# Kernel optimization log

Hardware: AMD Instinct MI355X
Metric: run time of the kernel (lower is better)

Reference implementation:

```python
import jax, jax.numpy as jnp
import numpy as np

EPS = 1e-6
H = 8        # num_heads
DH = 64      # head dim = embed_dim // num_heads
LN_EPS = 1e-5


def _layernorm(x, g, b):
    m = jnp.mean(x, axis=-1, keepdims=True)
    v = jnp.mean(jnp.square(x - m), axis=-1, keepdims=True)
    return (x - m) / jnp.sqrt(v + LN_EPS) * g + b


def _flow_attention(x, Wq, bq, Wk, bk, Wv, bv, Wo, bo):
    # Non-causal Flow-Attention (Flowformer): kernelized sigmoid Q/K,
    # flow-conservation sink/source normalization, linear-attention kv trick.
    B, L, D = x.shape
    S = L
    q = jax.nn.sigmoid((x @ Wq + bq).reshape(B, L, H, DH).transpose(0, 2, 1, 3))  # bhld
    k = jax.nn.sigmoid((x @ Wk + bk).reshape(B, S, H, DH).transpose(0, 2, 1, 3))
    v = (x @ Wv + bv).reshape(B, S, H, DH).transpose(0, 2, 1, 3)

    sink_incoming = 1.0 / jnp.einsum('nhld,nhd->nhl', q + EPS, k.sum(axis=2) + EPS)
    source_outgoing = 1.0 / jnp.einsum('nhld,nhd->nhl', k + EPS, q.sum(axis=2) + EPS)
    conserved_sink = jnp.einsum('nhld,nhd->nhl', q + EPS,
                                (k * source_outgoing[..., None]).sum(axis=2) + EPS)
    conserved_source = jnp.einsum('nhld,nhd->nhl', k + EPS,
                                  (q * sink_incoming[..., None]).sum(axis=2) + EPS)
    conserved_source = jnp.clip(conserved_source, -1.0, 1.0)
    sink_allocation = jax.nn.sigmoid(conserved_sink * (float(L) / float(S)))
    source_competition = jax.nn.softmax(conserved_source, axis=-1) * float(S)

    # linear attention: kv = k^T (v * comp), out = (q * sink_in) kv
    kv = jnp.einsum('nhld,nhlm->nhdm', k, v * source_competition[..., None])
    o = jnp.einsum('nhld,nhdm->nhlm', q * sink_incoming[..., None], kv)
    o = o * sink_allocation[..., None]
    o = o.transpose(0, 2, 1, 3).reshape(B, L, D)
    return o @ Wo + bo


def setup_inputs() -> dict:
    key = jax.random.key(0)
    ks = jax.random.split(key, 16)
    B, L, D, F = 2, 16384, 512, 2048
    s = 0.02
    inp = {
        'x': jax.random.normal(ks[0], (B, L, D), dtype=jnp.float32),
        'Wq': jax.random.normal(ks[1], (D, D), dtype=jnp.float32) * s,
        'bq': jnp.zeros((D,), jnp.float32),
        'Wk': jax.random.normal(ks[2], (D, D), dtype=jnp.float32) * s,
        'bk': jnp.zeros((D,), jnp.float32),
        'Wv': jax.random.normal(ks[3], (D, D), dtype=jnp.float32) * s,
        'bv': jnp.zeros((D,), jnp.float32),
        'Wo': jax.random.normal(ks[4], (D, D), dtype=jnp.float32) * s,
        'bo': jnp.zeros((D,), jnp.float32),
        'W1': jax.random.normal(ks[5], (D, F), dtype=jnp.float32) * s,
        'b1': jnp.zeros((F,), jnp.float32),
        'W2': jax.random.normal(ks[6], (F, D), dtype=jnp.float32) * s,
        'b2': jnp.zeros((D,), jnp.float32),
        'g1': jnp.ones((D,), jnp.float32),
        'be1': jnp.zeros((D,), jnp.float32),
        'g2': jnp.ones((D,), jnp.float32),
        'be2': jnp.zeros((D,), jnp.float32),
    }
    return inp


def reference(x, Wq, bq, Wk, bk, Wv, bv, Wo, bo, W1, b1, W2, b2, g1, be1, g2, be2):
    # norm_first FlowformerLayer. NOTE: original _sa_block returns
    # dropout(attn(x))[0, :, :] -> [L, D], broadcast-added over batch (faithful).
    sa = _flow_attention(_layernorm(x, g1, be1), Wq, bq, Wk, bk, Wv, bv, Wo, bo)[0]
    x = x + sa  # [B,L,D] + [L,D]
    h = _layernorm(x, g2, be2)
    h = jax.nn.gelu(h @ W1 + b1, approximate=False) @ W2 + b2
    return x + h
```

## Files before the change

### kernel.cpp

```cpp
#include <hip/hip_runtime.h>
#include <hip/hip_bf16.h>
#include <cstdint>
#include <cstddef>


#define L_SEQ 16384
#define EPSF 1e-6f

typedef __bf16 b16x8 __attribute__((ext_vector_type(8)));
typedef __bf16 b16x4 __attribute__((ext_vector_type(4)));
typedef float  f32x4 __attribute__((ext_vector_type(4)));

#define FENCE() asm volatile("" ::: "memory")
#define BARF()  { FENCE(); __builtin_amdgcn_s_barrier(); FENCE(); }
#define WAITV(n) asm volatile("s_waitcnt vmcnt(" #n ")" ::: "memory")

__device__ __forceinline__ void gload16(const void* g, void* l) {
  __builtin_amdgcn_global_load_lds((const __attribute__((address_space(1))) void*)g,
                                   (__attribute__((address_space(3))) void*)l, 16, 0, 0);
}

__device__ __forceinline__ float sigmoidf_(float x) { return 1.f / (1.f + __expf(-x)); }

__global__ __launch_bounds__(256) void convT(const float* __restrict__ src,
                                             __bf16* __restrict__ dst, int K, int N) {
  __shared__ float tile[32][33];
  const int k0 = blockIdx.y * 32, n0 = blockIdx.x * 32;
  const int tx = threadIdx.x & 31, ty = threadIdx.x >> 5;
#pragma unroll
  for (int i = 0; i < 32; i += 8) tile[ty + i][tx] = src[(size_t)(k0 + ty + i) * N + n0 + tx];
  __syncthreads();
#pragma unroll
  for (int i = 0; i < 32; i += 8)
    dst[(size_t)(n0 + ty + i) * K + k0 + tx] = (__bf16)tile[tx][ty + i];
}

__global__ __launch_bounds__(256) void biascat_k(const float* __restrict__ bq,
                                                 const float* __restrict__ bk,
                                                 const float* __restrict__ bv,
                                                 float* __restrict__ bc) {
  int i = blockIdx.x * 256 + threadIdx.x;
  bc[i] = (i < 512) ? bq[i] : (i < 1024) ? bk[i - 512] : bv[i - 1024];
}

__global__ __launch_bounds__(256) void zero_k(float* __restrict__ p, int n) {
  int i = blockIdx.x * 256 + threadIdx.x;
  if (i < n) p[i] = 0.f;
}

__global__ __launch_bounds__(128) void ln_rows(const float* __restrict__ x,
                                               const float* __restrict__ g,
                                               const float* __restrict__ be,
                                               __bf16* __restrict__ out) {
  const int row = blockIdx.x, t = threadIdx.x;
  const float4 xv = reinterpret_cast<const float4*>(x + (size_t)row * 512)[t];
  float s = xv.x + xv.y + xv.z + xv.w;
  float s2 = xv.x * xv.x + xv.y * xv.y + xv.z * xv.z + xv.w * xv.w;
#pragma unroll
  for (int off = 32; off > 0; off >>= 1) { s += __shfl_down(s, off); s2 += __shfl_down(s2, off); }
  __shared__ float red[4];
  if ((t & 63) == 0) { red[(t >> 6) * 2] = s; red[(t >> 6) * 2 + 1] = s2; }
  __syncthreads();
  const float S = red[0] + red[2], S2 = red[1] + red[3];
  const float mean = S * (1.f / 512.f);
  const float var = S2 * (1.f / 512.f) - mean * mean;
  const float inv = rsqrtf(var + 1e-5f);
  const float4 gv = reinterpret_cast<const float4*>(g)[t];
  const float4 bv = reinterpret_cast<const float4*>(be)[t];
  b16x4 o;
  o[0] = (__bf16)((xv.x - mean) * inv * gv.x + bv.x);
  o[1] = (__bf16)((xv.y - mean) * inv * gv.y + bv.y);
  o[2] = (__bf16)((xv.z - mean) * inv * gv.z + bv.z);
  o[3] = (__bf16)((xv.w - mean) * inv * gv.w + bv.w);
  reinterpret_cast<b16x4*>(out + (size_t)row * 512)[t] = o;
}

__global__ __launch_bounds__(128) void x2ln2_k(const float* __restrict__ x,
                                               const float* __restrict__ sa0,
                                               const float* __restrict__ sa1,
                                               const float* __restrict__ bo,
                                               const float* __restrict__ g,
                                               const float* __restrict__ be,
                                               float* __restrict__ xout,
                                               __bf16* __restrict__ lnout) {
  const int row = blockIdx.x, t = threadIdx.x;
  const int l = row & (L_SEQ - 1);
  float4 xv = reinterpret_cast<const float4*>(x + (size_t)row * 512)[t];
  const float4 s0 = reinterpret_cast<const float4*>(sa0 + (size_t)l * 512)[t];
  const float4 s1 = reinterpret_cast<const float4*>(sa1 + (size_t)l * 512)[t];
  const float4 bb = reinterpret_cast<const float4*>(bo)[t];
  xv.x += s0.x + s1.x + bb.x; xv.y += s0.y + s1.y + bb.y;
  xv.z += s0.z + s1.z + bb.z; xv.w += s0.w + s1.w + bb.w;
  reinterpret_cast<float4*>(xout + (size_t)row * 512)[t] = xv;
  float s = xv.x + xv.y + xv.z + xv.w;
  float s2 = xv.x * xv.x + xv.y * xv.y + xv.z * xv.z + xv.w * xv.w;
#pragma unroll
  for (int off = 32; off > 0; off >>= 1) { s += __shfl_down(s, off); s2 += __shfl_down(s2, off); }
  __shared__ float red[4];
  if ((t & 63) == 0) { red[(t >> 6) * 2] = s; red[(t >> 6) * 2 + 1] = s2; }
  __syncthreads();
  const float S = red[0] + red[2], S2 = red[1] + red[3];
  const float mean = S * (1.f / 512.f);
  const float var = S2 * (1.f / 512.f) - mean * mean;
  const float inv = rsqrtf(var + 1e-5f);
  const float4 gv = reinterpret_cast<const float4*>(g)[t];
  const float4 bv = reinterpret_cast<const float4*>(be)[t];
  b16x4 o;
  o[0] = (__bf16)((xv.x - mean) * inv * gv.x + bv.x);
  o[1] = (__bf16)((xv.y - mean) * inv * gv.y + bv.y);
  o[2] = (__bf16)((xv.z - mean) * inv * gv.z + bv.z);
  o[3] = (__bf16)((xv.w - mean) * inv * gv.w + bv.w);
  reinterpret_cast<b16x4*>(lnout + (size_t)row * 512)[t] = o;
}

template <int EPI, int KSPL>
__global__ __launch_bounds__(256, 4) void gemm128(const __bf16* __restrict__ A,
                                                  const __bf16* __restrict__ Bt,
                                                  const int M, const int N, const int K,
                                                  const float* __restrict__ bias,
                                                  float* __restrict__ f0,
                                                  __bf16* __restrict__ h0,
                                                  __bf16* __restrict__ h1,
                                                  float* __restrict__ f1,
                                                  float* __restrict__ f2) {
  __shared__ alignas(16) __bf16 lds[16384];

  if constexpr (KSPL) {
    const int z = blockIdx.y;
    A += (size_t)z * (K >> 1);
    Bt += (size_t)z * (K >> 1);
    f0 += (size_t)z * ((size_t)M * N);
  }
  const int nt = KSPL ? (K >> 6) : (K >> 5);

  const int nwg = gridDim.x;
  const int orig = blockIdx.x;
  const int cpx = nwg >> 3;
  const int wg = (orig & 7) * cpx + (orig >> 3);
  const int gx = N >> 7;
  const int bm = (wg / gx) << 7;
  const int bn = (wg % gx) << 7;

  const int t = threadIdx.x;
  const int w = t >> 6, lane = t & 63;
  const int wr = w >> 1, wc = w & 1;
  const int fr = lane & 15;
  const int kb = lane >> 4;

  const __bf16* As = A + (size_t)(bm + (t >> 2)) * K + (t & 3) * 8;
  const __bf16* Bs = Bt + (size_t)(bn + (t >> 2)) * K + (t & 3) * 8;

  f32x4 acc[4][4] = {};

  auto STG = [&](int s) {
    const int sel = (s & 1) * 4096;
    const __bf16* ap = As + (s << 5);
    const __bf16* bp = Bs + (s << 5);
    gload16(ap, &lds[sel + t * 8]);
    gload16(ap + (size_t)64 * K, &lds[sel + 2048 + t * 8]);
    gload16(bp, &lds[8192 + sel + t * 8]);
    gload16(bp + (size_t)64 * K, &lds[8192 + sel + 2048 + t * 8]);
  };

  STG(0);
  WAITV(0);
  BARF();

  for (int s = 0; s < nt; s++) {
    if (s + 1 < nt) STG(s + 1);
    const int ab = (s & 1) * 4096 + (wr * 64 + fr) * 32 + kb * 8;
    const int bb2 = 8192 + (s & 1) * 4096 + (wc * 64 + fr) * 32 + kb * 8;
    b16x8 av[4], bv[4];
#pragma unroll
    for (int m = 0; m < 4; m++)
      av[m] = *reinterpret_cast<const b16x8*>(&lds[ab + m * 512]);
#pragma unroll
    for (int n = 0; n < 4; n++)
      bv[n] = *reinterpret_cast<const b16x8*>(&lds[bb2 + n * 512]);
#pragma unroll
    for (int m = 0; m < 4; m++)
#pragma unroll
      for (int n = 0; n < 4; n++)
        acc[m][n] = __builtin_amdgcn_mfma_f32_16x16x32_bf16(av[m], bv[n], acc[m][n], 0, 0, 0);
    WAITV(0);
    BARF();
  }

  const int r0 = kb * 4;
  const int cc = fr;
  if constexpr (EPI == 0) {
    const int which = bn >> 9;
    float cs[4] = {0.f, 0.f, 0.f, 0.f};
#pragma unroll
    for (int m = 0; m < 4; m++) {
#pragma unroll
      for (int n = 0; n < 4; n++) {
        const int col = bn + wc * 64 + n * 16 + cc;
        const int c2 = col & 511;
#pragma unroll
        for (int r = 0; r < 4; r++) {
          const int row = bm + wr * 64 + m * 16 + r0 + r;
          float val = acc[m][n][r] + bias[col];
          if (which < 2) {
            val = sigmoidf_(val);
            cs[n] += val;
            ((which == 0) ? h0 : h1)[(size_t)row * 512 + c2] = (__bf16)val;
          } else {
            f0[(size_t)row * 512 + c2] = val;
          }
        }
      }
    }
    if (which < 2) {
      float* sums = (which == 0) ? f1 : f2;
#pragma unroll
      for (int n = 0; n < 4; n++) {
        float s = cs[n];
        s += __shfl_xor(s, 16);
        s += __shfl_xor(s, 32);
        if (kb == 0) atomicAdd(&sums[(bn & 511) + wc * 64 + n * 16 + cc], s);
      }
    }
  } else {
#pragma unroll
    for (int m = 0; m < 4; m++) {
#pragma unroll
      for (int n = 0; n < 4; n++) {
        const int col = bn + wc * 64 + n * 16 + cc;
#pragma unroll
        for (int r = 0; r < 4; r++) {
          const int row = bm + wr * 64 + m * 16 + r0 + r;
          float val = acc[m][n][r];
          if constexpr (EPI == 1) {
            f0[(size_t)row * N + col] = val;
          } else if constexpr (EPI == 2) {
            const float xg = val + bias[col];
            const float gel = 0.5f * xg * (1.f + erff(xg * 0.70710678118f));
            h0[(size_t)row * N + col] = (__bf16)gel;
          } else {
            const size_t idx = (size_t)row * N + col;
            f0[idx] = f0[idx] + val + bias[col];
          }
        }
      }
    }
  }
}

__global__ __launch_bounds__(256) void attn_pass1(const __bf16* __restrict__ q,
                                                  const __bf16* __restrict__ k,
                                                  const float* __restrict__ qsum,
                                                  const float* __restrict__ ksum,
                                                  float* __restrict__ si_out,
                                                  float* __restrict__ qkpart) {
  __shared__ float lsQ[512], lsK[512];
  const int t = threadIdx.x, lane = t & 63, wv = t >> 6;
  const int c0 = lane * 8;
  lsQ[t] = 0.f; lsQ[t + 256] = 0.f;
  lsK[t] = 0.f; lsK[t + 256] = 0.f;
  __syncthreads();
  float qs[8], ks[8];
#pragma unroll
  for (int j = 0; j < 8; j++) {
    qs[j] = qsum[c0 + j] + EPSF;
    ks[j] = ksum[c0 + j] + EPSF;
  }
  const int h = lane >> 3;
  float qacc[8] = {}, kacc[8] = {};
#pragma unroll 1
  for (int i = 0; i < 8; i++) {
    const int l = blockIdx.x * 32 + wv * 8 + i;
    const b16x8 q8 = *reinterpret_cast<const b16x8*>(q + (size_t)l * 512 + c0);
    const b16x8 k8 = *reinterpret_cast<const b16x8*>(k + (size_t)l * 512 + c0);
    float qf[8], kf[8];
    float p1 = 0.f, p2 = 0.f;
#pragma unroll
    for (int j = 0; j < 8; j++) {
      qf[j] = (float)q8[j]; kf[j] = (float)k8[j];
      p1 += (qf[j] + EPSF) * ks[j];
      p2 += (kf[j] + EPSF) * qs[j];
    }
    p1 += __shfl_xor(p1, 1); p2 += __shfl_xor(p2, 1);
    p1 += __shfl_xor(p1, 2); p2 += __shfl_xor(p2, 2);
    p1 += __shfl_xor(p1, 4); p2 += __shfl_xor(p2, 4);
    const float siv = 1.f / p1, sov = 1.f / p2;
    if ((lane & 7) == 0) si_out[h * L_SEQ + l] = siv;
#pragma unroll
    for (int j = 0; j < 8; j++) { qacc[j] += qf[j] * siv; kacc[j] += kf[j] * sov; }
  }
#pragma unroll
  for (int j = 0; j < 8; j++) {
    atomicAdd(&lsQ[c0 + j], qacc[j]);
    atomicAdd(&lsK[c0 + j], kacc[j]);
  }
  __syncthreads();
  float* qp = qkpart + (size_t)blockIdx.x * 1024;
  qp[t] = lsQ[t];
  qp[t + 256] = lsQ[t + 256];
  qp[t + 512] = lsK[t];
  qp[t + 768] = lsK[t + 256];
}

__global__ __launch_bounds__(256) void reduce_qk(const float* __restrict__ qkpart,
                                                 float* __restrict__ outv) {
  const int i = blockIdx.x * 256 + threadIdx.x;
  float s = 0.f;
#pragma unroll 4
  for (int b = 0; b < 512; b++) s += qkpart[(size_t)b * 1024 + i];
  outv[i] = s;
}

__global__ __launch_bounds__(256) void kv_part(const __bf16* __restrict__ k,
                                               const float* __restrict__ v,
                                               const float* __restrict__ qsi,
                                               float* __restrict__ kvpart,
                                               float* __restrict__ separt) {
  const int h = blockIdx.y, bx = blockIdx.x, t = threadIdx.x;
  __shared__ float lsK[64 * 68];
  __shared__ float lsV[64 * 68];
  __shared__ float lsRed[256];
  const int r = t >> 2, cq = (t & 3) * 16;
  float qv[16];
#pragma unroll
  for (int j = 0; j < 16; j++) qv[j] = qsi[h * 64 + cq + j] + EPSF;
  const int d = t & 63, mg = t >> 6;
  f32x4 acc4[4] = {};
  float seloc = 0.f;
#pragma unroll 1
  for (int sc = 0; sc < 4; sc++) {
    const int l = bx * 256 + sc * 64 + r;
    __syncthreads();
    const b16x8 k8a = *reinterpret_cast<const b16x8*>(k + (size_t)l * 512 + h * 64 + cq);
    const b16x8 k8b = *reinterpret_cast<const b16x8*>(k + (size_t)l * 512 + h * 64 + cq + 8);
    f32x4 v4[4];
#pragma unroll
    for (int jj = 0; jj < 4; jj++)
      v4[jj] = *reinterpret_cast<const f32x4*>(v + (size_t)l * 512 + h * 64 + cq + jj * 4);
    float kf[16];
#pragma unroll
    for (int j = 0; j < 8; j++) { kf[j] = (float)k8a[j]; kf[8 + j] = (float)k8b[j]; }
    float p = 0.f;
#pragma unroll
    for (int j = 0; j < 16; j++) p += (kf[j] + EPSF) * qv[j];
    p += __shfl_xor(p, 1);
    p += __shfl_xor(p, 2);
    p = fminf(fmaxf(p, -1.f), 1.f);
    const float ce = __expf(p);
    if ((t & 3) == 0) seloc += ce;
#pragma unroll
    for (int j = 0; j < 16; j++) lsK[r * 68 + cq + j] = kf[j];
#pragma unroll
    for (int jj = 0; jj < 4; jj++)
      *reinterpret_cast<f32x4*>(&lsV[r * 68 + cq + jj * 4]) = v4[jj] * ce;
    __syncthreads();
    for (int rr = 0; rr < 64; rr++) {
      const float kd = lsK[rr * 68 + d];
      const f32x4* lv = reinterpret_cast<const f32x4*>(&lsV[rr * 68 + mg * 16]);
#pragma unroll
      for (int jj = 0; jj < 4; jj++) acc4[jj] += lv[jj] * kd;
    }
  }
  float* kp = kvpart + ((size_t)h * 64 + bx) * 4096;
#pragma unroll
  for (int jj = 0; jj < 4; jj++)
    *reinterpret_cast<f32x4*>(&kp[d * 64 + mg * 16 + jj * 4]) = acc4[jj];
  lsRed[t] = ((t & 3) == 0) ? seloc : 0.f;
  __syncthreads();
  for (int s2 = 128; s2 > 0; s2 >>= 1) {
    if (t < s2) lsRed[t] += lsRed[t + s2];
    __syncthreads();
  }
  if (t == 0) separt[h * 64 + bx] = lsRed[0];
}

__global__ __launch_bounds__(256) void kv_reduce(const float* __restrict__ kvpart,
                                                 const float* __restrict__ separt,
                                                 float* __restrict__ kvout,
                                                 float* __restrict__ sumexp) {
  const int h = blockIdx.y, t = threadIdx.x;
  const int i = blockIdx.x * 256 + t;
  float s = 0.f;
#pragma unroll 4
  for (int b = 0; b < 64; b++) s += kvpart[((size_t)h * 64 + b) * 4096 + i];
  kvout[h * 4096 + i] = s;
  if (blockIdx.x == 0 && t < 64) {
    float e = separt[h * 64 + t];
#pragma unroll
    for (int off2 = 32; off2 > 0; off2 >>= 1) e += __shfl_down(e, off2);
    if (t == 0) sumexp[h] = e;
  }
}

__global__ __launch_bounds__(256) void o_kernel(const __bf16* __restrict__ q,
                                                const float* __restrict__ kvin,
                                                const float* __restrict__ si,
                                                const float* __restrict__ kso,
                                                const float* __restrict__ sumexp,
                                                __bf16* __restrict__ o) {
  const int h = blockIdx.y;
  const int l0 = blockIdx.x * 32;
  const int t = threadIdx.x;
  __shared__ float lsKV[64 * 64];
  __shared__ float lsQ[32 * 65];
  __shared__ float lsF[32];
  const float Sfac = (float)L_SEQ / sumexp[h];
#pragma unroll
  for (int j = 0; j < 16; j++) lsKV[t + j * 256] = kvin[h * 4096 + t + j * 256];
  const int r = t >> 3, c8 = (t & 7) * 8;
  float ksov[8];
#pragma unroll
  for (int j = 0; j < 8; j++) ksov[j] = kso[h * 64 + c8 + j] + EPSF;
  const b16x8 q8 = *reinterpret_cast<const b16x8*>(q + (size_t)(l0 + r) * 512 + h * 64 + c8);
  float p = 0.f;
#pragma unroll
  for (int j = 0; j < 8; j++) {
    const float qf = (float)q8[j];
    lsQ[r * 65 + c8 + j] = qf;
    p += (qf + EPSF) * ksov[j];
  }
  p += __shfl_xor(p, 1);
  p += __shfl_xor(p, 2);
  p += __shfl_xor(p, 4);
  if ((t & 7) == 0) lsF[r] = sigmoidf_(p) * si[h * L_SEQ + l0 + r] * Sfac;
  __syncthreads();
  const int m = t & 63, rg = t >> 6;
#pragma unroll 1
  for (int i = 0; i < 8; i++) {
    const int rr = rg + i * 4;
    float a = 0.f;
#pragma unroll
    for (int dd = 0; dd < 64; dd++) a += lsQ[rr * 65 + dd] * lsKV[dd * 64 + m];
    o[(size_t)(l0 + rr) * 512 + h * 64 + m] = (__bf16)(a * lsF[rr]);
  }
}

extern "C" void kernel_launch(void* const* d_in, const int* in_sizes, int n_in,
                              void* d_out, int out_size, void* d_ws, size_t ws_size,
                              hipStream_t stream) {
  const float* x  = (const float*)d_in[0];
  const float* Wq = (const float*)d_in[1];
  const float* bq = (const float*)d_in[2];
  const float* Wk = (const float*)d_in[3];
  const float* bk = (const float*)d_in[4];
  const float* Wv = (const float*)d_in[5];
  const float* bv = (const float*)d_in[6];
  const float* Wo = (const float*)d_in[7];
  const float* bo = (const float*)d_in[8];
  const float* W1 = (const float*)d_in[9];
  const float* b1 = (const float*)d_in[10];
  const float* W2 = (const float*)d_in[11];
  const float* b2 = (const float*)d_in[12];
  const float* g1 = (const float*)d_in[13];
  const float* be1 = (const float*)d_in[14];
  const float* g2 = (const float*)d_in[15];
  const float* be2 = (const float*)d_in[16];
  float* out = (float*)d_out;

  char* ws = (char*)d_ws;
  size_t off = 0;
  auto alloc = [&](size_t bytes) -> char* {
    char* p = ws + off;
    off += (bytes + 255) & ~(size_t)255;
    return p;
  };

  char* regA = alloc(134217728);
  __bf16* ln1  = (__bf16*)regA;
  __bf16* qb16 = (__bf16*)(regA + 16777216);
  __bf16* kb16 = (__bf16*)(regA + 33554432);
  float*  vb   = (float*)(regA + 50331648);
  __bf16* ob   = (__bf16*)(regA + 83886080);
  float*  sa   = (float*)regA;
  __bf16* act  = (__bf16*)regA;

  __bf16* ln2 = (__bf16*)alloc((size_t)32768 * 512 * 2);
  __bf16* Wqkvt = (__bf16*)alloc((size_t)1536 * 512 * 2);
  __bf16* Wot = (__bf16*)alloc((size_t)512 * 512 * 2);
  __bf16* W1t = (__bf16*)alloc((size_t)2048 * 512 * 2);
  __bf16* W2t = (__bf16*)alloc((size_t)512 * 2048 * 2);
  float* biascat = (float*)alloc(1536 * 4);
  float* si = (float*)alloc((size_t)8 * L_SEQ * 4);
  float* stats = (float*)alloc(34880 * 4);
  float* qsum = stats;
  float* ksum = stats + 512;
  float* qsi = stats + 1024;
  float* kso = stats + 1536;
  float* sumexp = stats + 2048;
  float* kvbuf = stats + 2112;
  float* kvpart = (float*)alloc((size_t)8 * 64 * 4096 * 4);
  float* separt = (float*)alloc(512 * 4);
  float* qkpart = (float*)alloc((size_t)512 * 1024 * 4);

  convT<<<dim3(16, 16), 256, 0, stream>>>(Wq, Wqkvt, 512, 512);
  convT<<<dim3(16, 16), 256, 0, stream>>>(Wk, Wqkvt + (size_t)512 * 512, 512, 512);
  convT<<<dim3(16, 16), 256, 0, stream>>>(Wv, Wqkvt + (size_t)1024 * 512, 512, 512);
  convT<<<dim3(16, 16), 256, 0, stream>>>(Wo, Wot, 512, 512);
  convT<<<dim3(64, 16), 256, 0, stream>>>(W1, W1t, 512, 2048);
  convT<<<dim3(16, 64), 256, 0, stream>>>(W2, W2t, 2048, 512);
  biascat_k<<<6, 256, 0, stream>>>(bq, bk, bv, biascat);
  zero_k<<<(2112 + 255) / 256, 256, 0, stream>>>(stats, 2112);

  ln_rows<<<L_SEQ, 128, 0, stream>>>(x, g1, be1, ln1);
  gemm128<0, 0><<<1536, 256, 0, stream>>>(ln1, Wqkvt, L_SEQ, 1536, 512,
                                          biascat, vb, qb16, kb16, qsum, ksum);

  attn_pass1<<<512, 256, 0, stream>>>(qb16, kb16, qsum, ksum, si, qkpart);
  reduce_qk<<<4, 256, 0, stream>>>(qkpart, qsi);
  kv_part<<<dim3(64, 8), 256, 0, stream>>>(kb16, vb, qsi, kvpart, separt);
  kv_reduce<<<dim3(16, 8), 256, 0, stream>>>(kvpart, separt, kvbuf, sumexp);
  o_kernel<<<dim3(L_SEQ / 32, 8), 256, 0, stream>>>(qb16, kvbuf, si, kso, sumexp, ob);

  gemm128<1, 1><<<dim3(512, 2), 256, 0, stream>>>(ob, Wot, L_SEQ, 512, 512,
                                                  nullptr, sa, nullptr, nullptr,
                                                  nullptr, nullptr);

  x2ln2_k<<<2 * L_SEQ, 128, 0, stream>>>(x, sa, sa + (size_t)L_SEQ * 512, bo,
                                         g2, be2, out, ln2);

  gemm128<2, 0><<<4096, 256, 0, stream>>>(ln2, W1t, 2 * L_SEQ, 2048, 512,
                                          b1, nullptr, act, nullptr, nullptr, nullptr);
  gemm128<3, 0><<<1024, 256, 0, stream>>>(act, W2t, 2 * L_SEQ, 512, 2048,
                                          b2, out, nullptr, nullptr, nullptr, nullptr);
}
```

Before: 514.0 us.

## Triple-buffer GEMM LDS staging and XOR-swizzle tiles to avoid bank conflicts

Moves the bf16 GEMM main loop from double-buffered to triple-buffered global-to-LDS loads, prefetching two K-steps ahead with partial vmcnt waits, so memory latency overlaps with MFMA work. It also applies an XOR swizzle to the 16-byte chunk position within each LDS row, on both the load and read sides, to reduce LDS bank conflicts. LDS per block grows from 32KB to 48KB and launch bounds drop to 3 blocks per CU, trading occupancy for deeper prefetch.

```diff
diff --git a/kernel.cpp b/kernel.cpp
--- a/kernel.cpp
+++ b/kernel.cpp
@@ -114,7 +114,7 @@
 }
 
 template <int EPI, int KSPL>
-__global__ __launch_bounds__(256, 4) void gemm128(const __bf16* __restrict__ A,
+__global__ __launch_bounds__(256, 3) void gemm128(const __bf16* __restrict__ A,
                                                   const __bf16* __restrict__ Bt,
                                                   const int M, const int N, const int K,
                                                   const float* __restrict__ bias,
@@ -123,7 +123,7 @@
                                                   __bf16* __restrict__ h1,
                                                   float* __restrict__ f1,
                                                   float* __restrict__ f2) {
-  __shared__ alignas(16) __bf16 lds[16384];
+  __shared__ alignas(16) __bf16 lds[24576];
 
   if constexpr (KSPL) {
     const int z = blockIdx.y;
@@ -146,30 +146,35 @@
   const int wr = w >> 1, wc = w & 1;
   const int fr = lane & 15;
   const int kb = lane >> 4;
-
-  const __bf16* As = A + (size_t)(bm + (t >> 2)) * K + (t & 3) * 8;
-  const __bf16* Bs = Bt + (size_t)(bn + (t >> 2)) * K + (t & 3) * 8;
+  const int swo = (kb ^ (fr & 3)) * 8;
+
+  const int srow = t >> 2;
+  const int sxz = (t & 3) ^ (srow & 3);
+  const __bf16* As = A + (size_t)(bm + srow) * K + sxz * 8;
+  const __bf16* Bs = Bt + (size_t)(bn + srow) * K + sxz * 8;
 
   f32x4 acc[4][4] = {};
 
-  auto STG = [&](int s) {
-    const int sel = (s & 1) * 4096;
+  auto STG = [&](int s, int buf) {
+    const int sel = buf * 8192;
     const __bf16* ap = As + (s << 5);
     const __bf16* bp = Bs + (s << 5);
     gload16(ap, &lds[sel + t * 8]);
     gload16(ap + (size_t)64 * K, &lds[sel + 2048 + t * 8]);
-    gload16(bp, &lds[8192 + sel + t * 8]);
-    gload16(bp + (size_t)64 * K, &lds[8192 + sel + 2048 + t * 8]);
+    gload16(bp, &lds[sel + 4096 + t * 8]);
+    gload16(bp + (size_t)64 * K, &lds[sel + 6144 + t * 8]);
   };
 
-  STG(0);
-  WAITV(0);
+  STG(0, 0);
+  if (nt > 1) STG(1, 1);
+  WAITV(4);
   BARF();
 
+  int bc = 0, bs = 2;
   for (int s = 0; s < nt; s++) {
-    if (s + 1 < nt) STG(s + 1);
-    const int ab = (s & 1) * 4096 + (wr * 64 + fr) * 32 + kb * 8;
-    const int bb2 = 8192 + (s & 1) * 4096 + (wc * 64 + fr) * 32 + kb * 8;
+    if (s + 2 < nt) STG(s + 2, bs);
+    const int ab = bc * 8192 + (wr * 64 + fr) * 32 + swo;
+    const int bb2 = bc * 8192 + 4096 + (wc * 64 + fr) * 32 + swo;
     b16x8 av[4], bv[4];
 #pragma unroll
     for (int m = 0; m < 4; m++)
@@ -182,8 +187,11 @@
 #pragma unroll
       for (int n = 0; n < 4; n++)
         acc[m][n] = __builtin_amdgcn_mfma_f32_16x16x32_bf16(av[m], bv[n], acc[m][n], 0, 0, 0);
-    WAITV(0);
+    if (s + 2 < nt) { WAITV(4); }
+    else if (s + 1 < nt) { WAITV(0); }
     BARF();
+    bc = (bc == 2) ? 0 : bc + 1;
+    bs = (bs == 2) ? 0 : bs + 1;
   }
 
   const int r0 = kb * 4;
```

Measured after the change: 527.7 us. 2.7% more time.

## Deepen GEMM LDS pipeline to four stages with remapped LDS layout

Applied to the files above, without the earlier changes.

Replaces the double-buffered K loop in the bf16 GEMM with a four-buffer pipeline that keeps three stages of global-to-LDS loads in flight, waiting only on the oldest. It also remaps which rows each lane loads and how fragments are addressed in LDS, likely to cut bank conflicts. LDS use doubles and launch bounds drop to two blocks per CU, trading occupancy for more latency hiding. The unrolled loop assumes the number of K tiles is a multiple of four.

```diff
diff --git a/kernel.cpp b/kernel.cpp
--- a/kernel.cpp
+++ b/kernel.cpp
@@ -114,7 +114,7 @@
 }
 
 template <int EPI, int KSPL>
-__global__ __launch_bounds__(256, 4) void gemm128(const __bf16* __restrict__ A,
+__global__ __launch_bounds__(256, 2) void gemm128(const __bf16* __restrict__ A,
                                                   const __bf16* __restrict__ Bt,
                                                   const int M, const int N, const int K,
                                                   const float* __restrict__ bias,
@@ -123,7 +123,7 @@
                                                   __bf16* __restrict__ h1,
                                                   float* __restrict__ f1,
                                                   float* __restrict__ f2) {
-  __shared__ alignas(16) __bf16 lds[16384];
+  __shared__ alignas(16) __bf16 lds[32768];
 
   if constexpr (KSPL) {
     const int z = blockIdx.y;
@@ -147,44 +147,62 @@
   const int fr = lane & 15;
   const int kb = lane >> 4;
 
-  const __bf16* As = A + (size_t)(bm + (t >> 2)) * K + (t & 3) * 8;
-  const __bf16* Bs = Bt + (size_t)(bn + (t >> 2)) * K + (t & 3) * 8;
+  const int lrow = 2 * (lane >> 3) + ((lane >> 2) & 1);
+  const __bf16* Asrc = A + (size_t)(bm + w * 32 + lrow) * K + (lane & 3) * 8;
+  const __bf16* Bsrc = Bt + (size_t)(bn + w * 32 + lrow) * K + (lane & 3) * 8;
+  const int dA = w * 1024 + lane * 8;
+  const int dB = 4096 + dA;
+
+  const int fro = (fr & 1) * 32 + kb * 8;
+  const int arb = (wr * 32 + (fr >> 1)) * 64 + fro;
+  const int brb = 4096 + (wc * 32 + (fr >> 1)) * 64 + fro;
 
   f32x4 acc[4][4] = {};
 
-  auto STG = [&](int s) {
-    const int sel = (s & 1) * 4096;
-    const __bf16* ap = As + (s << 5);
-    const __bf16* bp = Bs + (s << 5);
-    gload16(ap, &lds[sel + t * 8]);
-    gload16(ap + (size_t)64 * K, &lds[sel + 2048 + t * 8]);
-    gload16(bp, &lds[8192 + sel + t * 8]);
-    gload16(bp + (size_t)64 * K, &lds[8192 + sel + 2048 + t * 8]);
+  auto STG = [&](int s, int buf) {
+    const int base = buf * 8192;
+    const __bf16* ap = Asrc + (s << 5);
+    const __bf16* bp = Bsrc + (s << 5);
+    gload16(ap, &lds[base + dA]);
+    gload16(ap + (size_t)16 * K, &lds[base + dA + 512]);
+    gload16(bp, &lds[base + dB]);
+    gload16(bp + (size_t)16 * K, &lds[base + dB + 512]);
   };
 
-  STG(0);
-  WAITV(0);
+#define GITER(ss, buf)                                                        \
+  {                                                                           \
+    const int s_ = (ss);                                                      \
+    if (s_ + 3 < nt) STG(s_ + 3, ((buf) + 3) & 3);                            \
+    const int ab = (buf) * 8192 + arb;                                        \
+    const int bb2 = (buf) * 8192 + brb;                                       \
+    b16x8 av[4], bv[4];                                                       \
+    _Pragma("unroll") for (int m = 0; m < 4; m++)                             \
+        av[m] = *reinterpret_cast<const b16x8*>(&lds[ab + m * 512]);          \
+    _Pragma("unroll") for (int n = 0; n < 4; n++)                             \
+        bv[n] = *reinterpret_cast<const b16x8*>(&lds[bb2 + n * 512]);         \
+    _Pragma("unroll") for (int m = 0; m < 4; m++)                             \
+        _Pragma("unroll") for (int n = 0; n < 4; n++) acc[m][n] =             \
+        __builtin_amdgcn_mfma_f32_16x16x32_bf16(av[m], bv[n], acc[m][n],      \
+                                                0, 0, 0);                     \
+    if (s_ + 3 < nt) { WAITV(8); }                                            \
+    else if (s_ + 2 < nt) { WAITV(4); }                                       \
+    else if (s_ + 1 < nt) { WAITV(0); }                                       \
+    BARF();                                                                   \
+  }
+
+  STG(0, 0);
+  STG(1, 1);
+  STG(2, 2);
+  WAITV(8);
   BARF();
 
-  for (int s = 0; s < nt; s++) {
-    if (s + 1 < nt) STG(s + 1);
-    const int ab = (s & 1) * 4096 + (wr * 64 + fr) * 32 + kb * 8;
-    const int bb2 = 8192 + (s & 1) * 4096 + (wc * 64 + fr) * 32 + kb * 8;
-    b16x8 av[4], bv[4];
-#pragma unroll
-    for (int m = 0; m < 4; m++)
-      av[m] = *reinterpret_cast<const b16x8*>(&lds[ab + m * 512]);
-#pragma unroll
-    for (int n = 0; n < 4; n++)
-      bv[n] = *reinterpret_cast<const b16x8*>(&lds[bb2 + n * 512]);
-#pragma unroll
-    for (int m = 0; m < 4; m++)
-#pragma unroll
-      for (int n = 0; n < 4; n++)
-        acc[m][n] = __builtin_amdgcn_mfma_f32_16x16x32_bf16(av[m], bv[n], acc[m][n], 0, 0, 0);
-    WAITV(0);
-    BARF();
-  }
+  for (int s = 0; s < nt; s += 4) {
+    GITER(s, 0);
+    GITER(s + 1, 1);
+    GITER(s + 2, 2);
+    GITER(s + 3, 3);
+  }
+#undef GITER
 
   const int r0 = kb * 4;
   const int cc = fr;
```

After: 565.1 us. 1.1x slower.

## Switch GEMM to 32x32x16 MFMA with K=64 tiles and XOR-swizzled LDS

Applied to the files above, without the earlier changes.

Rewrites the bf16 GEMM mainloop to use 32x32x16 MFMA instructions instead of 16x16x32, doubles the K step per stage to 64, and XOR-swizzles the LDS layout to avoid bank conflicts on fragment reads. LDS use doubles to 64 KB, so the occupancy hint drops from 4 to 2 blocks per CU. The aim is fewer LDS reads per MFMA, fewer barriers per K, and conflict-free shared memory access, at the cost of lower occupancy and more LDS per block. Epilogues are remapped to the 32x32 accumulator layout.

```diff
diff --git a/kernel.cpp b/kernel.cpp
--- a/kernel.cpp
+++ b/kernel.cpp
@@ -10,6 +10,7 @@
 typedef __bf16 b16x8 __attribute__((ext_vector_type(8)));
 typedef __bf16 b16x4 __attribute__((ext_vector_type(4)));
 typedef float  f32x4 __attribute__((ext_vector_type(4)));
+typedef float  f32x16 __attribute__((ext_vector_type(16)));
 
 #define FENCE() asm volatile("" ::: "memory")
 #define BARF()  { FENCE(); __builtin_amdgcn_s_barrier(); FENCE(); }
@@ -114,7 +115,7 @@
 }
 
 template <int EPI, int KSPL>
-__global__ __launch_bounds__(256, 4) void gemm128(const __bf16* __restrict__ A,
+__global__ __launch_bounds__(256, 2) void gemm128(const __bf16* __restrict__ A,
                                                   const __bf16* __restrict__ Bt,
                                                   const int M, const int N, const int K,
                                                   const float* __restrict__ bias,
@@ -123,7 +124,7 @@
                                                   __bf16* __restrict__ h1,
                                                   float* __restrict__ f1,
                                                   float* __restrict__ f2) {
-  __shared__ alignas(16) __bf16 lds[16384];
+  __shared__ alignas(16) __bf16 lds[32768];
 
   if constexpr (KSPL) {
     const int z = blockIdx.y;
@@ -131,7 +132,7 @@
     Bt += (size_t)z * (K >> 1);
     f0 += (size_t)z * ((size_t)M * N);
   }
-  const int nt = KSPL ? (K >> 6) : (K >> 5);
+  const int nt = KSPL ? (K >> 7) : (K >> 6);
 
   const int nwg = gridDim.x;
   const int orig = blockIdx.x;
@@ -144,63 +145,66 @@
   const int t = threadIdx.x;
   const int w = t >> 6, lane = t & 63;
   const int wr = w >> 1, wc = w & 1;
-  const int fr = lane & 15;
-  const int kb = lane >> 4;
-
-  const __bf16* As = A + (size_t)(bm + (t >> 2)) * K + (t & 3) * 8;
-  const __bf16* Bs = Bt + (size_t)(bn + (t >> 2)) * K + (t & 3) * 8;
-
-  f32x4 acc[4][4] = {};
-
-  auto STG = [&](int s) {
-    const int sel = (s & 1) * 4096;
-    const __bf16* ap = As + (s << 5);
-    const __bf16* bp = Bs + (s << 5);
-    gload16(ap, &lds[sel + t * 8]);
-    gload16(ap + (size_t)64 * K, &lds[sel + 2048 + t * 8]);
-    gload16(bp, &lds[8192 + sel + t * 8]);
-    gload16(bp + (size_t)64 * K, &lds[8192 + sel + 2048 + t * 8]);
+  const int l31 = lane & 31, l5 = lane >> 5, l7 = lane & 7;
+
+  const int sr = t >> 3;
+  const int sc = (t & 7) ^ (sr & 7);
+  const __bf16* Asrc = A + (size_t)(bm + sr) * K + sc * 8;
+  const __bf16* Bsrc = Bt + (size_t)(bn + sr) * K + sc * 8;
+  const int dst0 = t * 8;
+
+  f32x16 acc[2][2] = {};
+
+  auto STG = [&](int s, int buf) {
+    const int base = buf * 16384;
+    const __bf16* ap = Asrc + (s << 6);
+    const __bf16* bp = Bsrc + (s << 6);
+#pragma unroll
+    for (int j = 0; j < 4; j++) {
+      gload16(ap + (size_t)(j << 5) * K, &lds[base + dst0 + (j << 11)]);
+      gload16(bp + (size_t)(j << 5) * K, &lds[base + 8192 + dst0 + (j << 11)]);
+    }
   };
 
-  STG(0);
+  STG(0, 0);
   WAITV(0);
   BARF();
 
+  int cur = 0;
   for (int s = 0; s < nt; s++) {
-    if (s + 1 < nt) STG(s + 1);
-    const int ab = (s & 1) * 4096 + (wr * 64 + fr) * 32 + kb * 8;
-    const int bb2 = 8192 + (s & 1) * 4096 + (wc * 64 + fr) * 32 + kb * 8;
-    b16x8 av[4], bv[4];
-#pragma unroll
-    for (int m = 0; m < 4; m++)
-      av[m] = *reinterpret_cast<const b16x8*>(&lds[ab + m * 512]);
-#pragma unroll
-    for (int n = 0; n < 4; n++)
-      bv[n] = *reinterpret_cast<const b16x8*>(&lds[bb2 + n * 512]);
-#pragma unroll
-    for (int m = 0; m < 4; m++)
-#pragma unroll
-      for (int n = 0; n < 4; n++)
-        acc[m][n] = __builtin_amdgcn_mfma_f32_16x16x32_bf16(av[m], bv[n], acc[m][n], 0, 0, 0);
+    if (s + 1 < nt) STG(s + 1, cur ^ 1);
+    const int abase = cur * 16384 + (wr * 64 + l31) * 64;
+    const int bbase = cur * 16384 + 8192 + (wc * 64 + l31) * 64;
+#pragma unroll
+    for (int ks = 0; ks < 4; ks++) {
+      const int slot = ((ks * 2 + l5) ^ l7) * 8;
+      const b16x8 a0 = *reinterpret_cast<const b16x8*>(&lds[abase + slot]);
+      const b16x8 a1 = *reinterpret_cast<const b16x8*>(&lds[abase + 2048 + slot]);
+      const b16x8 b0 = *reinterpret_cast<const b16x8*>(&lds[bbase + slot]);
+      const b16x8 b1 = *reinterpret_cast<const b16x8*>(&lds[bbase + 2048 + slot]);
+      acc[0][0] = __builtin_amdgcn_mfma_f32_32x32x16_bf16(a0, b0, acc[0][0], 0, 0, 0);
+      acc[0][1] = __builtin_amdgcn_mfma_f32_32x32x16_bf16(a0, b1, acc[0][1], 0, 0, 0);
+      acc[1][0] = __builtin_amdgcn_mfma_f32_32x32x16_bf16(a1, b0, acc[1][0], 0, 0, 0);
+      acc[1][1] = __builtin_amdgcn_mfma_f32_32x32x16_bf16(a1, b1, acc[1][1], 0, 0, 0);
+    }
     WAITV(0);
     BARF();
-  }
-
-  const int r0 = kb * 4;
-  const int cc = fr;
+    cur ^= 1;
+  }
+
   if constexpr (EPI == 0) {
     const int which = bn >> 9;
-    float cs[4] = {0.f, 0.f, 0.f, 0.f};
-#pragma unroll
-    for (int m = 0; m < 4; m++) {
-#pragma unroll
-      for (int n = 0; n < 4; n++) {
-        const int col = bn + wc * 64 + n * 16 + cc;
+    float cs[2] = {0.f, 0.f};
+#pragma unroll
+    for (int m = 0; m < 2; m++) {
+#pragma unroll
+      for (int n = 0; n < 2; n++) {
+        const int col = bn + wc * 64 + n * 32 + l31;
         const int c2 = col & 511;
 #pragma unroll
-        for (int r = 0; r < 4; r++) {
-          const int row = bm + wr * 64 + m * 16 + r0 + r;
-          float val = acc[m][n][r] + bias[col];
+        for (int j = 0; j < 16; j++) {
+          const int row = bm + wr * 64 + m * 32 + (j & 3) + 8 * (j >> 2) + 4 * l5;
+          float val = acc[m][n][j] + bias[col];
           if (which < 2) {
             val = sigmoidf_(val);
             cs[n] += val;
@@ -214,23 +218,22 @@
     if (which < 2) {
       float* sums = (which == 0) ? f1 : f2;
 #pragma unroll
-      for (int n = 0; n < 4; n++) {
+      for (int n = 0; n < 2; n++) {
         float s = cs[n];
-        s += __shfl_xor(s, 16);
         s += __shfl_xor(s, 32);
-        if (kb == 0) atomicAdd(&sums[(bn & 511) + wc * 64 + n * 16 + cc], s);
+        if (l5 == 0) atomicAdd(&sums[(bn & 511) + wc * 64 + n * 32 + l31], s);
       }
     }
   } else {
 #pragma unroll
-    for (int m = 0; m < 4; m++) {
-#pragma unroll
-      for (int n = 0; n < 4; n++) {
-        const int col = bn + wc * 64 + n * 16 + cc;
-#pragma unroll
-        for (int r = 0; r < 4; r++) {
-          const int row = bm + wr * 64 + m * 16 + r0 + r;
-          float val = acc[m][n][r];
+    for (int m = 0; m < 2; m++) {
+#pragma unroll
+      for (int n = 0; n < 2; n++) {
+        const int col = bn + wc * 64 + n * 32 + l31;
+#pragma unroll
+        for (int j = 0; j < 16; j++) {
+          const int row = bm + wr * 64 + m * 32 + (j & 3) + 8 * (j >> 2) + 4 * l5;
+          float val = acc[m][n][j];
           if constexpr (EPI == 1) {
             f0[(size_t)row * N + col] = val;
           } else if constexpr (EPI == 2) {
```

After: 572.9 us. +11.5%, slower.
